# Kernel tuning notes

Hardware: AMD Instinct MI355X
Metric: run time of the kernel (lower is better)

## Reference

```python
import jax, jax.numpy as jnp
import numpy as np

N_EMBD = 768
N_HEAD = 12


def setup_inputs() -> dict:
    key = jax.random.key(0)
    ks = jax.random.split(key, 5)
    B, T, C = 8, 1024, N_EMBD
    s_in = 1.0 / np.sqrt(C)
    x = jax.random.normal(ks[0], (B, T, C), dtype=jnp.float32)
    w_attn = jax.random.normal(ks[1], (C, 3 * C), dtype=jnp.float32) * s_in
    b_attn = jnp.zeros((3 * C,), dtype=jnp.float32)
    w_proj = jax.random.normal(ks[2], (C, C), dtype=jnp.float32) * s_in
    b_proj = jnp.zeros((C,), dtype=jnp.float32)
    return {"x": x, "w_attn": w_attn, "b_attn": b_attn,
            "w_proj": w_proj, "b_proj": b_proj}


def reference(x, w_attn, b_attn, w_proj, b_proj):
    B, T, C = x.shape
    H, hs = N_HEAD, C // N_HEAD
    qkv = x @ w_attn + b_attn                      # [B,T,3C]
    q, k, v = jnp.split(qkv, 3, axis=-1)
    # [B,H,T,hs]
    q = q.reshape(B, T, H, hs).transpose(0, 2, 1, 3)
    k = k.reshape(B, T, H, hs).transpose(0, 2, 1, 3)
    v = v.reshape(B, T, H, hs).transpose(0, 2, 1, 3)
    att = jnp.einsum('bhqd,bhkd->bhqk', q, k) * (1.0 / np.sqrt(hs))
    causal = jnp.tril(jnp.ones((T, T), dtype=bool))
    att = jnp.where(causal, att, -jnp.inf)
    att = jax.nn.softmax(att, axis=-1)
    y = jnp.einsum('bhqk,bhkd->bhqd', att, v)      # [B,H,T,hs]
    y = y.transpose(0, 2, 1, 3).reshape(B, T, C)
    return y @ w_proj + b_proj
```

## Files before the change

### kernel.cpp

```cpp
#include <hip/hip_runtime.h>
#include <hip/hip_bf16.h>
#include <stdint.h>

typedef unsigned short u16;
typedef short short8 __attribute__((ext_vector_type(8)));
typedef short short4v __attribute__((ext_vector_type(4)));
typedef float floatx4 __attribute__((ext_vector_type(4)));

__device__ __forceinline__ float b2f(u16 v) {
  union { unsigned int u; float f; } c; c.u = ((unsigned int)v) << 16; return c.f;
}
__device__ __forceinline__ u16 f2b(float f) {
  union { float f; unsigned int u; } c; c.f = f;
  unsigned int u = c.u;
  return (u16)((u + 0x7fffu + ((u >> 16) & 1u)) >> 16);
}

__device__ __forceinline__ void gld_lds16(const u16* g, u16* l) {
  __builtin_amdgcn_global_load_lds(
      (const __attribute__((address_space(1))) unsigned int*)g,
      (__attribute__((address_space(3))) unsigned int*)l,
      16, 0, 0);
}

__device__ __forceinline__ void tile_transpose_f2b(
    const float* __restrict__ in, u16* __restrict__ out,
    int inRS, int outRS, int rb, int cb, int tid)
{
  __shared__ __align__(16) u16 t[64][72];
  const int r = tid >> 2, sg = tid & 3;
  const float* ip = in + (long)(rb + r) * inRS + cb + sg * 16;
#pragma unroll
  for (int i = 0; i < 16; i += 4) {
    float4 f = *(const float4*)(ip + i);
    t[r][sg * 16 + i]     = f2b(f.x);
    t[r][sg * 16 + i + 1] = f2b(f.y);
    t[r][sg * 16 + i + 2] = f2b(f.z);
    t[r][sg * 16 + i + 3] = f2b(f.w);
  }
  __syncthreads();
  short8 v0, v1;
#pragma unroll
  for (int i = 0; i < 8; i++) v0[i] = (short)t[sg * 16 + i][r];
#pragma unroll
  for (int i = 0; i < 8; i++) v1[i] = (short)t[sg * 16 + 8 + i][r];
  *(short8*)(out + (long)(cb + r) * outRS + rb + sg * 16)     = v0;
  *(short8*)(out + (long)(cb + r) * outRS + rb + sg * 16 + 8) = v1;
}

__global__ __launch_bounds__(256) void prep(
    const float* __restrict__ x, u16* __restrict__ xb,
    const float* __restrict__ w_attn, u16* __restrict__ wTa,
    const float* __restrict__ w_proj, u16* __restrict__ wTp)
{
  const int bid = blockIdx.x, tid = threadIdx.x;
  if (bid < 6144) {
    int i = (bid * 256 + tid) * 4;
    float4 f = *(const float4*)(x + i);
    short4v v;
    v[0] = (short)f2b(f.x); v[1] = (short)f2b(f.y);
    v[2] = (short)f2b(f.z); v[3] = (short)f2b(f.w);
    *(short4v*)(xb + i) = v;
  } else if (bid < 6576) {
    int t = bid - 6144;
    tile_transpose_f2b(w_attn, wTa, 2304, 768, (t / 36) * 64, (t % 36) * 64, tid);
  } else {
    int t = bid - 6576;
    tile_transpose_f2b(w_proj, wTp, 768, 768, (t / 12) * 64, (t % 12) * 64, tid);
  }
}

__device__ __forceinline__ void store_out(u16* p, float v)  { *p = f2b(v); }
__device__ __forceinline__ void store_out(float* p, float v) { *p = v; }

template <int BM>
__device__ __forceinline__ void stage(
    const u16* __restrict__ A, const u16* __restrict__ Bt,
    long rowbase, long colbase, int K, int k0,
    u16* dA, u16* dB, int tid)
{
  const int c0 = tid, c1 = tid + 256;
  const int ar0 = c0 >> 2, ak0 = (c0 & 3) * 8;
  const int ar1 = c1 >> 2, ak1 = (c1 & 3) * 8;
  gld_lds16(A + (rowbase + ar0) * K + k0 + ak0, dA + c0 * 8);
  if (BM == 128)
    gld_lds16(A + (rowbase + ar1) * K + k0 + ak1, dA + c1 * 8);
  gld_lds16(Bt + (colbase + ar0) * K + k0 + ak0, dB + c0 * 8);
  gld_lds16(Bt + (colbase + ar1) * K + k0 + ak1, dB + c1 * 8);
}

template <typename OT, int BM, bool SPLIT>
__global__ __launch_bounds__(256) void gemm_bt_bias(
    const u16* __restrict__ A, const u16* __restrict__ Bt,
    const float* __restrict__ bias, OT* __restrict__ C, u16* __restrict__ vT,
    int M, int N, int K, int strideC)
{
  constexpr int WNF = (BM == 128) ? 4 : 2;
  __shared__ __align__(16) u16 sA[2][BM * 32];
  __shared__ __align__(16) u16 sB[2][128 * 32];
  const int tid = threadIdx.x;
  const int lane = tid & 63;
  const int wave = tid >> 6;
  const int wm = (BM == 128) ? (wave >> 1) * 64 : 0;
  const int wn = (BM == 128) ? (wave & 1) * 64 : wave * 32;
  const int l15 = lane & 15;
  const int q = lane >> 4;
  const long rowbase = (long)blockIdx.y * BM;
  const long colbase = (long)blockIdx.x * 128;

  floatx4 acc[4][WNF];
#pragma unroll
  for (int i = 0; i < 4; i++)
#pragma unroll
    for (int j = 0; j < WNF; j++) acc[i][j] = (floatx4){0.f, 0.f, 0.f, 0.f};

  stage<BM>(A, Bt, rowbase, colbase, K, 0, sA[0], sB[0], tid);
  __syncthreads();

  const int NIT = K / 32;
  for (int it = 0; it < NIT; ++it) {
    const int cur = it & 1;
    if (it + 1 < NIT)
      stage<BM>(A, Bt, rowbase, colbase, K, (it + 1) * 32, sA[cur ^ 1], sB[cur ^ 1], tid);
    short8 af[4], bf[WNF];
#pragma unroll
    for (int mt = 0; mt < 4; mt++)
      af[mt] = *(const short8*)(sA[cur] + (wm + mt * 16 + l15) * 32 + q * 8);
#pragma unroll
    for (int nt = 0; nt < WNF; nt++)
      bf[nt] = *(const short8*)(sB[cur] + (wn + nt * 16 + l15) * 32 + q * 8);
#pragma unroll
    for (int mt = 0; mt < 4; mt++)
#pragma unroll
      for (int nt = 0; nt < WNF; nt++)
        acc[mt][nt] = __builtin_amdgcn_mfma_f32_16x16x32_bf16(af[mt], bf[nt], acc[mt][nt], 0, 0, 0);
    if (it + 1 < NIT) __syncthreads();
  }

  if (SPLIT && colbase >= 1536) {
    const long b = rowbase >> 10;
    const int t0b = (int)(rowbase & 1023) + wm;
#pragma unroll
    for (int nt = 0; nt < WNF; nt++) {
      const int col = (int)colbase + wn + nt * 16 + l15;
      const float bv = bias[col];
      const int dloc = col - 1536;
      u16* bp = vT + (b * 12 + (dloc >> 6)) * 65536L + (long)(dloc & 63) * 1024;
#pragma unroll
      for (int mt = 0; mt < 4; mt++) {
        short4v pv;
#pragma unroll
        for (int r = 0; r < 4; r++) pv[r] = (short)f2b(acc[mt][nt][r] + bv);
        *(short4v*)(bp + t0b + mt * 16 + q * 4) = pv;
      }
    }
  } else {
#pragma unroll
    for (int nt = 0; nt < WNF; nt++) {
      const long col = colbase + wn + nt * 16 + l15;
      const float bv = bias[col];
#pragma unroll
      for (int mt = 0; mt < 4; mt++)
#pragma unroll
        for (int r = 0; r < 4; r++) {
          const long row = rowbase + wm + mt * 16 + q * 4 + r;
          store_out(C + row * strideC + col, acc[mt][nt][r] + bv);
        }
    }
  }
}

#define QKV_K 768
#define QKV_NT 24
#define VMW(n) asm volatile("s_waitcnt vmcnt(" #n ")" ::: "memory")

__global__ __launch_bounds__(768, 3) void gemm_qkv_288(
    const u16* __restrict__ A, const u16* __restrict__ Bt,
    const float* __restrict__ bias, u16* __restrict__ qkOut, u16* __restrict__ vT)
{
  __shared__ __align__(16) u16 sA[4][256 * 32];
  __shared__ __align__(16) u16 sB[4][288 * 32];

  const int bid = blockIdx.x;
  const int wg = (bid & 7) * 32 + (bid >> 3);
  const int bx = wg & 7;
  const int by = wg >> 3;

  const int tid = threadIdx.x;
  const int lane = tid & 63;
  const int l15 = lane & 15, q = lane >> 4;
  const int wave = tid >> 6;
  const int wm = (wave / 6) * 128;
  const int wn = (wave % 6) * 48;
  const long rowbase = (long)by * 256;
  const long colbase = (long)bx * 288;
  const int xq = ((q ^ ((l15 >> 1) & 3)) << 3);

  const int cA0 = tid, cA1 = 768 + tid;
  const int cB0 = tid, cB1 = 768 + tid;
  const u16* pa0 = A + (rowbase + (cA0 >> 2)) * QKV_K + ((((cA0 & 3) ^ ((cA0 >> 3) & 3))) << 3);
  const u16* pa1 = A + (rowbase + (cA1 >> 2)) * QKV_K + ((((cA1 & 3) ^ ((cA1 >> 3) & 3))) << 3);
  const u16* pb0 = Bt + (colbase + (cB0 >> 2)) * QKV_K + ((((cB0 & 3) ^ ((cB0 >> 3) & 3))) << 3);
  const u16* pb1 = Bt + (colbase + (cB1 >> 2)) * QKV_K + ((((cB1 & 3) ^ ((cB1 >> 3) & 3))) << 3);
  const bool hasA1 = (tid < 256);
  const bool hasB1 = (tid < 384);

#define STAGE(t, s) do { \
    const long k0_ = (long)(t) * 32; \
    gld_lds16(pa0 + k0_, &sA[s][cA0 * 8]); \
    if (hasA1) gld_lds16(pa1 + k0_, &sA[s][cA1 * 8]); \
    gld_lds16(pb0 + k0_, &sB[s][cB0 * 8]); \
    if (hasB1) gld_lds16(pb1 + k0_, &sB[s][cB1 * 8]); } while (0)

  floatx4 acc[8][3];
#pragma unroll
  for (int i = 0; i < 8; i++)
#pragma unroll
    for (int n = 0; n < 3; n++) acc[i][n] = (floatx4){0.f, 0.f, 0.f, 0.f};

  STAGE(0, 0); STAGE(1, 1); STAGE(2, 2);
  if (wave < 4) VMW(8); else if (wave < 6) VMW(6); else VMW(4);
  __builtin_amdgcn_s_barrier();

#pragma unroll 4
  for (int j = 0; j < QKV_NT; ++j) {
    const int slot = j & 3;
    const u16* ap = sA[slot];
    const u16* bp = sB[slot];

    short8 bf[3];
#pragma unroll
    for (int nt = 0; nt < 3; nt++)
      bf[nt] = *(const short8*)(bp + (wn + nt * 16 + l15) * 32 + xq);
    short8 af[4];
#pragma unroll
    for (int mt = 0; mt < 4; mt++)
      af[mt] = *(const short8*)(ap + (wm + mt * 16 + l15) * 32 + xq);
    if (j + 3 < QKV_NT) STAGE(j + 3, (j + 3) & 3);
    __builtin_amdgcn_s_barrier();
    __builtin_amdgcn_s_setprio(1);
#pragma unroll
    for (int mt = 0; mt < 4; mt++)
#pragma unroll
      for (int nt = 0; nt < 3; nt++)
        acc[mt][nt] = __builtin_amdgcn_mfma_f32_16x16x32_bf16(af[mt], bf[nt], acc[mt][nt], 0, 0, 0);
    __builtin_amdgcn_s_setprio(0);

#pragma unroll
    for (int mt = 0; mt < 4; mt++)
      af[mt] = *(const short8*)(ap + (wm + 64 + mt * 16 + l15) * 32 + xq);
    __builtin_amdgcn_s_setprio(1);
#pragma unroll
    for (int mt = 0; mt < 4; mt++)
#pragma unroll
      for (int nt = 0; nt < 3; nt++)
        acc[4 + mt][nt] = __builtin_amdgcn_mfma_f32_16x16x32_bf16(af[mt], bf[nt], acc[4 + mt][nt], 0, 0, 0);
    __builtin_amdgcn_s_setprio(0);

    if (j < QKV_NT - 1) {
      if (j + 3 < QKV_NT) {
        if (wave < 4) VMW(8); else if (wave < 6) VMW(6); else VMW(4);
      } else if (j + 2 < QKV_NT) {
        if (wave < 4) VMW(4); else if (wave < 6) VMW(3); else VMW(2);
      } else {
        VMW(0);
      }
      __builtin_amdgcn_s_barrier();
    }
  }
#undef STAGE

#pragma unroll
  for (int nt = 0; nt < 3; nt++) {
    const int fragc = (int)colbase + wn + nt * 16;
    const int col = fragc + l15;
    const float bv = bias[col];
    if (fragc >= 1536) {
      const long bb = rowbase >> 10;
      const int dloc = col - 1536;
      u16* op = vT + (bb * 12 + (dloc >> 6)) * 65536L + (long)(dloc & 63) * 1024;
      const int t0 = (int)(rowbase & 1023) + wm;
#pragma unroll
      for (int mt = 0; mt < 8; mt++) {
        short4v pv;
#pragma unroll
        for (int r = 0; r < 4; r++) pv[r] = (short)f2b(acc[mt][nt][r] + bv);
        *(short4v*)(op + t0 + mt * 16 + q * 4) = pv;
      }
    } else {
#pragma unroll
      for (int mt = 0; mt < 8; mt++)
#pragma unroll
        for (int r = 0; r < 4; r++) {
          const long row = rowbase + wm + mt * 16 + q * 4 + r;
          qkOut[row * 1536 + col] = f2b(acc[mt][nt][r] + bv);
        }
    }
  }
}
#undef VMW

__global__ __launch_bounds__(256) void attn_fwd(
    const u16* __restrict__ qk, const u16* __restrict__ vT, u16* __restrict__ y)
{
  const int bh = blockIdx.x;
  const int qt = 15 - blockIdx.y;
  const int b = bh / 12, h = bh % 12;
  const long rowOff = (long)b * 1024;
  const int qb = qt * 64;

  __shared__ __align__(16) u16 sK[64 * 72];
  __shared__ __align__(16) u16 sV[2][64 * 72];
  __shared__ __align__(16) u16 sP[64 * 72];

  const int tid = threadIdx.x;
  const int lane = tid & 63, wave = tid >> 6;
  const int l15 = lane & 15, q = lane >> 4;
  const int qrow_g = qb + wave * 16 + l15;

  short8 qf[2];
  {
    const u16* qp = qk + (long)(rowOff + qrow_g) * 1536 + h * 64 + q * 8;
    short8 a0 = *(const short8*)(qp);
    short8 a1 = *(const short8*)(qp + 32);
#pragma unroll
    for (int i = 0; i < 8; i++) {
      a0[i] = (short)f2b(b2f((u16)a0[i]) * 0.125f);
      a1[i] = (short)f2b(b2f((u16)a1[i]) * 0.125f);
    }
    qf[0] = a0; qf[1] = a1;
  }

  float m_i = -1e30f, l_i = 0.f;
  floatx4 o[4];
#pragma unroll
  for (int nt = 0; nt < 4; nt++) o[nt] = (floatx4){0.f, 0.f, 0.f, 0.f};

  for (int j = 0; j <= qt; j++) {
    const int jb = j * 64;
    u16* sVc = sV[j & 1];
#pragma unroll
    for (int rep = 0; rep < 2; rep++) {
      int idx = tid + rep * 256;
      int r = idx >> 3, ch = (idx & 7) * 8;
      *(short8*)(sK + r * 72 + ch) =
          *(const short8*)(qk + (long)(rowOff + jb + r) * 1536 + 768 + h * 64 + ch);
      *(short8*)(sVc + r * 72 + ch) =
          *(const short8*)(vT + (long)bh * 65536 + (long)r * 1024 + jb + ch);
    }
    __syncthreads();

    floatx4 sf[4];
#pragma unroll
    for (int mt = 0; mt < 4; mt++) sf[mt] = (floatx4){0.f, 0.f, 0.f, 0.f};
#pragma unroll
    for (int kk = 0; kk < 2; kk++) {
#pragma unroll
      for (int mt = 0; mt < 4; mt++) {
        short8 kf = *(const short8*)(sK + (mt * 16 + l15) * 72 + kk * 32 + q * 8);
        sf[mt] = __builtin_amdgcn_mfma_f32_16x16x32_bf16(kf, qf[kk], sf[mt], 0, 0, 0);
      }
    }

    float mx = m_i;
#pragma unroll
    for (int mt = 0; mt < 4; mt++)
#pragma unroll
      for (int r = 0; r < 4; r++) {
        int key_g = jb + mt * 16 + q * 4 + r;
        float v = sf[mt][r];
        if (key_g > qrow_g) v = -1e30f;
        sf[mt][r] = v;
        mx = fmaxf(mx, v);
      }
    mx = fmaxf(mx, __shfl_xor(mx, 16));
    mx = fmaxf(mx, __shfl_xor(mx, 32));
    float al = __expf(m_i - mx);
    m_i = mx;
    float rsum = 0.f;
#pragma unroll
    for (int mt = 0; mt < 4; mt++) {
      short4v pv;
#pragma unroll
      for (int r = 0; r < 4; r++) {
        float p = __expf(sf[mt][r] - mx);
        rsum += p;
        pv[r] = (short)f2b(p);
      }
      *(short4v*)(sP + (wave * 16 + l15) * 72 + mt * 16 + q * 4) = pv;
    }
    rsum += __shfl_xor(rsum, 16);
    rsum += __shfl_xor(rsum, 32);
    l_i = l_i * al + rsum;
    __syncthreads();

    float al_r[4];
#pragma unroll
    for (int r = 0; r < 4; r++) al_r[r] = __shfl(al, q * 4 + r);
#pragma unroll
    for (int nt = 0; nt < 4; nt++)
#pragma unroll
      for (int r = 0; r < 4; r++) o[nt][r] *= al_r[r];
#pragma unroll
    for (int kk = 0; kk < 2; kk++) {
      short8 pf = *(const short8*)(sP + (wave * 16 + l15) * 72 + kk * 32 + q * 8);
#pragma unroll
      for (int nt = 0; nt < 4; nt++) {
        short8 vf = *(const short8*)(sVc + (nt * 16 + l15) * 72 + kk * 32 + q * 8);
        o[nt] = __builtin_amdgcn_mfma_f32_16x16x32_bf16(pf, vf, o[nt], 0, 0, 0);
      }
    }
  }

  float linv = 1.f / l_i;
  float li_r[4];
#pragma unroll
  for (int r = 0; r < 4; r++) li_r[r] = __shfl(linv, q * 4 + r);
#pragma unroll
  for (int nt = 0; nt < 4; nt++)
#pragma unroll
    for (int r = 0; r < 4; r++) {
      int row = qb + wave * 16 + q * 4 + r;
      int col = h * 64 + nt * 16 + l15;
      y[(rowOff + row) * 768 + col] = f2b(o[nt][r] * li_r[r]);
    }
}

extern "C" void kernel_launch(void* const* d_in, const int* in_sizes, int n_in,
                              void* d_out, int out_size, void* d_ws, size_t ws_size,
                              hipStream_t stream) {
  const float* x      = (const float*)d_in[0];
  const float* w_attn = (const float*)d_in[1];
  const float* b_attn = (const float*)d_in[2];
  const float* w_proj = (const float*)d_in[3];
  const float* b_proj = (const float*)d_in[4];
  float* out = (float*)d_out;

  char* ws = (char*)d_ws;
  u16* xb   = (u16*)ws; ws += (size_t)8192 * 768 * 2;
  u16* wTa  = (u16*)ws; ws += (size_t)2304 * 768 * 2;
  u16* wTp  = (u16*)ws; ws += (size_t)768 * 768 * 2;
  u16* qk   = (u16*)ws; ws += (size_t)8192 * 1536 * 2;
  u16* vT   = (u16*)ws; ws += (size_t)96 * 64 * 1024 * 2;
  u16* yatt = (u16*)ws; ws += (size_t)8192 * 768 * 2;

  prep<<<dim3(6720), 256, 0, stream>>>(x, xb, w_attn, wTa, w_proj, wTp);

  gemm_qkv_288<<<dim3(256), 768, 0, stream>>>(xb, wTa, b_attn, qk, vT);

  attn_fwd<<<dim3(96, 16), 256, 0, stream>>>(qk, vT, yatt);

  gemm_bt_bias<float, 128, false><<<dim3(6, 64), 256, 0, stream>>>(
      yatt, wTp, b_proj, out, (u16*)nullptr, 8192, 768, 768, 768);
}
```

Before: 196.7 us.

## Use 128-row query tiles with register-prefetched K/V in attention; drop a GEMM barrier

The attention kernel now runs 8 waves per block over a 128-row query tile, so each K/V tile loaded to shared memory serves twice as many query rows. The next K/V tile is loaded into registers while the current tile is computed, then written to shared memory after the first sync. Waves whose rows lie entirely before a causal key tile skip that tile's work. Separately, one s_barrier in the QKV GEMM main loop is removed to cut synchronisation, which risks a shared-memory reuse race if no other barrier guards the staging slots.

```diff
diff --git a/kernel.cpp b/kernel.cpp
--- a/kernel.cpp
+++ b/kernel.cpp
@@ -237,7 +237,6 @@
     for (int mt = 0; mt < 4; mt++)
       af[mt] = *(const short8*)(ap + (wm + mt * 16 + l15) * 32 + xq);
     if (j + 3 < QKV_NT) STAGE(j + 3, (j + 3) & 3);
-    __builtin_amdgcn_s_barrier();
     __builtin_amdgcn_s_setprio(1);
 #pragma unroll
     for (int mt = 0; mt < 4; mt++)
@@ -300,23 +299,29 @@
 }
 #undef VMW
 
-__global__ __launch_bounds__(256) void attn_fwd(
+__global__ __launch_bounds__(512) void attn_fwd(
     const u16* __restrict__ qk, const u16* __restrict__ vT, u16* __restrict__ y)
 {
   const int bh = blockIdx.x;
-  const int qt = 15 - blockIdx.y;
+  const int qt = 7 - blockIdx.y;
   const int b = bh / 12, h = bh % 12;
   const long rowOff = (long)b * 1024;
-  const int qb = qt * 64;
+  const int qb = qt * 128;
 
   __shared__ __align__(16) u16 sK[64 * 72];
   __shared__ __align__(16) u16 sV[2][64 * 72];
-  __shared__ __align__(16) u16 sP[64 * 72];
+  __shared__ __align__(16) u16 sP[128 * 72];
 
   const int tid = threadIdx.x;
   const int lane = tid & 63, wave = tid >> 6;
   const int l15 = lane & 15, q = lane >> 4;
-  const int qrow_g = qb + wave * 16 + l15;
+  const int qrow_l = wave * 16 + l15;
+  const int qrow_g = qb + qrow_l;
+  const int wave_max_row = qb + wave * 16 + 15;
+
+  const int sr = tid >> 3, sc = (tid & 7) * 8;
+  const u16* kBase = qk + rowOff * 1536 + 768 + (long)h * 64;
+  const u16* vBase = vT + (long)bh * 65536;
 
   short8 qf[2];
   {
@@ -336,80 +341,94 @@
 #pragma unroll
   for (int nt = 0; nt < 4; nt++) o[nt] = (floatx4){0.f, 0.f, 0.f, 0.f};
 
-  for (int j = 0; j <= qt; j++) {
+  const int J = 2 * qt + 1;
+
+  *(short8*)(sK + sr * 72 + sc)    = *(const short8*)(kBase + (long)sr * 1536 + sc);
+  *(short8*)(sV[0] + sr * 72 + sc) = *(const short8*)(vBase + (long)sr * 1024 + sc);
+  __syncthreads();
+
+  for (int j = 0; j <= J; j++) {
     const int jb = j * 64;
-    u16* sVc = sV[j & 1];
-#pragma unroll
-    for (int rep = 0; rep < 2; rep++) {
-      int idx = tid + rep * 256;
-      int r = idx >> 3, ch = (idx & 7) * 8;
-      *(short8*)(sK + r * 72 + ch) =
-          *(const short8*)(qk + (long)(rowOff + jb + r) * 1536 + 768 + h * 64 + ch);
-      *(short8*)(sVc + r * 72 + ch) =
-          *(const short8*)(vT + (long)bh * 65536 + (long)r * 1024 + jb + ch);
+    const bool active = (jb <= wave_max_row);
+    const u16* sVc = sV[j & 1];
+
+    short8 rk = {}, rv = {};
+    if (j < J) {
+      rk = *(const short8*)(kBase + (long)(jb + 64 + sr) * 1536 + sc);
+      rv = *(const short8*)(vBase + (long)sr * 1024 + (jb + 64) + sc);
+    }
+
+    float al = 1.f;
+    if (active) {
+      floatx4 sf[4];
+#pragma unroll
+      for (int mt = 0; mt < 4; mt++) sf[mt] = (floatx4){0.f, 0.f, 0.f, 0.f};
+#pragma unroll
+      for (int kk = 0; kk < 2; kk++) {
+#pragma unroll
+        for (int mt = 0; mt < 4; mt++) {
+          short8 kf = *(const short8*)(sK + (mt * 16 + l15) * 72 + kk * 32 + q * 8);
+          sf[mt] = __builtin_amdgcn_mfma_f32_16x16x32_bf16(kf, qf[kk], sf[mt], 0, 0, 0);
+        }
+      }
+
+      float mx = m_i;
+#pragma unroll
+      for (int mt = 0; mt < 4; mt++)
+#pragma unroll
+        for (int r = 0; r < 4; r++) {
+          int key_g = jb + mt * 16 + q * 4 + r;
+          float v = sf[mt][r];
+          if (key_g > qrow_g) v = -1e30f;
+          sf[mt][r] = v;
+          mx = fmaxf(mx, v);
+        }
+      mx = fmaxf(mx, __shfl_xor(mx, 16));
+      mx = fmaxf(mx, __shfl_xor(mx, 32));
+      al = __expf(m_i - mx);
+      m_i = mx;
+      float rsum = 0.f;
+#pragma unroll
+      for (int mt = 0; mt < 4; mt++) {
+        short4v pv;
+#pragma unroll
+        for (int r = 0; r < 4; r++) {
+          float p = __expf(sf[mt][r] - mx);
+          rsum += p;
+          pv[r] = (short)f2b(p);
+        }
+        *(short4v*)(sP + qrow_l * 72 + mt * 16 + q * 4) = pv;
+      }
+      rsum += __shfl_xor(rsum, 16);
+      rsum += __shfl_xor(rsum, 32);
+      l_i = l_i * al + rsum;
     }
     __syncthreads();
 
-    floatx4 sf[4];
-#pragma unroll
-    for (int mt = 0; mt < 4; mt++) sf[mt] = (floatx4){0.f, 0.f, 0.f, 0.f};
-#pragma unroll
-    for (int kk = 0; kk < 2; kk++) {
-#pragma unroll
-      for (int mt = 0; mt < 4; mt++) {
-        short8 kf = *(const short8*)(sK + (mt * 16 + l15) * 72 + kk * 32 + q * 8);
-        sf[mt] = __builtin_amdgcn_mfma_f32_16x16x32_bf16(kf, qf[kk], sf[mt], 0, 0, 0);
-      }
-    }
-
-    float mx = m_i;
-#pragma unroll
-    for (int mt = 0; mt < 4; mt++)
-#pragma unroll
-      for (int r = 0; r < 4; r++) {
-        int key_g = jb + mt * 16 + q * 4 + r;
-        float v = sf[mt][r];
-        if (key_g > qrow_g) v = -1e30f;
-        sf[mt][r] = v;
-        mx = fmaxf(mx, v);
-      }
-    mx = fmaxf(mx, __shfl_xor(mx, 16));
-    mx = fmaxf(mx, __shfl_xor(mx, 32));
-    float al = __expf(m_i - mx);
-    m_i = mx;
-    float rsum = 0.f;
-#pragma unroll
-    for (int mt = 0; mt < 4; mt++) {
-      short4v pv;
-#pragma unroll
-      for (int r = 0; r < 4; r++) {
-        float p = __expf(sf[mt][r] - mx);
-        rsum += p;
-        pv[r] = (short)f2b(p);
-      }
-      *(short4v*)(sP + (wave * 16 + l15) * 72 + mt * 16 + q * 4) = pv;
-    }
-    rsum += __shfl_xor(rsum, 16);
-    rsum += __shfl_xor(rsum, 32);
-    l_i = l_i * al + rsum;
+    if (j < J) {
+      *(short8*)(sK + sr * 72 + sc)            = rk;
+      *(short8*)(sV[(j + 1) & 1] + sr * 72 + sc) = rv;
+    }
+
+    if (active) {
+      float al_r[4];
+#pragma unroll
+      for (int r = 0; r < 4; r++) al_r[r] = __shfl(al, q * 4 + r);
+#pragma unroll
+      for (int nt = 0; nt < 4; nt++)
+#pragma unroll
+        for (int r = 0; r < 4; r++) o[nt][r] *= al_r[r];
+#pragma unroll
+      for (int kk = 0; kk < 2; kk++) {
+        short8 pf = *(const short8*)(sP + qrow_l * 72 + kk * 32 + q * 8);
+#pragma unroll
+        for (int nt = 0; nt < 4; nt++) {
+          short8 vf = *(const short8*)(sVc + (nt * 16 + l15) * 72 + kk * 32 + q * 8);
+          o[nt] = __builtin_amdgcn_mfma_f32_16x16x32_bf16(pf, vf, o[nt], 0, 0, 0);
+        }
+      }
+    }
     __syncthreads();
-
-    float al_r[4];
-#pragma unroll
-    for (int r = 0; r < 4; r++) al_r[r] = __shfl(al, q * 4 + r);
-#pragma unroll
-    for (int nt = 0; nt < 4; nt++)
-#pragma unroll
-      for (int r = 0; r < 4; r++) o[nt][r] *= al_r[r];
-#pragma unroll
-    for (int kk = 0; kk < 2; kk++) {
-      short8 pf = *(const short8*)(sP + (wave * 16 + l15) * 72 + kk * 32 + q * 8);
-#pragma unroll
-      for (int nt = 0; nt < 4; nt++) {
-        short8 vf = *(const short8*)(sVc + (nt * 16 + l15) * 72 + kk * 32 + q * 8);
-        o[nt] = __builtin_amdgcn_mfma_f32_16x16x32_bf16(pf, vf, o[nt], 0, 0, 0);
-      }
-    }
   }
 
   float linv = 1.f / l_i;
@@ -448,7 +467,7 @@
 
   gemm_qkv_288<<<dim3(256), 768, 0, stream>>>(xb, wTa, b_attn, qk, vT);
 
-  attn_fwd<<<dim3(96, 16), 256, 0, stream>>>(qk, vT, yatt);
+  attn_fwd<<<dim3(96, 8), 512, 0, stream>>>(qk, vT, yatt);
 
   gemm_bt_bias<float, 128, false><<<dim3(6, 64), 256, 0, stream>>>(
       yatt, wTp, b_proj, out, (u16*)nullptr, 8192, 768, 768, 768);
```

Measured after the change: 188.8 us. -4.0%, faster.

## Replace projection GEMM with 4-stage 256x96 pipelined kernel, drop extra QKV barrier

Applied to the files above, without the earlier changes.

The output projection now uses a dedicated 768-thread kernel with 256x96 tiles, a 4-slot global-to-LDS ring with swizzled layout, and per-wave vmcnt waits, replacing the generic double-buffered 128x128 GEMM. It also removes a redundant mid-iteration barrier in the QKV GEMM loop. The aim is better overlap of loads and MFMA work and less synchronisation. The risk is a race if the removed barrier was needed for slot reuse.

```diff
diff --git a/kernel.cpp b/kernel.cpp
--- a/kernel.cpp
+++ b/kernel.cpp
@@ -70,106 +70,6 @@
   }
 }
 
-__device__ __forceinline__ void store_out(u16* p, float v)  { *p = f2b(v); }
-__device__ __forceinline__ void store_out(float* p, float v) { *p = v; }
-
-template <int BM>
-__device__ __forceinline__ void stage(
-    const u16* __restrict__ A, const u16* __restrict__ Bt,
-    long rowbase, long colbase, int K, int k0,
-    u16* dA, u16* dB, int tid)
-{
-  const int c0 = tid, c1 = tid + 256;
-  const int ar0 = c0 >> 2, ak0 = (c0 & 3) * 8;
-  const int ar1 = c1 >> 2, ak1 = (c1 & 3) * 8;
-  gld_lds16(A + (rowbase + ar0) * K + k0 + ak0, dA + c0 * 8);
-  if (BM == 128)
-    gld_lds16(A + (rowbase + ar1) * K + k0 + ak1, dA + c1 * 8);
-  gld_lds16(Bt + (colbase + ar0) * K + k0 + ak0, dB + c0 * 8);
-  gld_lds16(Bt + (colbase + ar1) * K + k0 + ak1, dB + c1 * 8);
-}
-
-template <typename OT, int BM, bool SPLIT>
-__global__ __launch_bounds__(256) void gemm_bt_bias(
-    const u16* __restrict__ A, const u16* __restrict__ Bt,
-    const float* __restrict__ bias, OT* __restrict__ C, u16* __restrict__ vT,
-    int M, int N, int K, int strideC)
-{
-  constexpr int WNF = (BM == 128) ? 4 : 2;
-  __shared__ __align__(16) u16 sA[2][BM * 32];
-  __shared__ __align__(16) u16 sB[2][128 * 32];
-  const int tid = threadIdx.x;
-  const int lane = tid & 63;
-  const int wave = tid >> 6;
-  const int wm = (BM == 128) ? (wave >> 1) * 64 : 0;
-  const int wn = (BM == 128) ? (wave & 1) * 64 : wave * 32;
-  const int l15 = lane & 15;
-  const int q = lane >> 4;
-  const long rowbase = (long)blockIdx.y * BM;
-  const long colbase = (long)blockIdx.x * 128;
-
-  floatx4 acc[4][WNF];
-#pragma unroll
-  for (int i = 0; i < 4; i++)
-#pragma unroll
-    for (int j = 0; j < WNF; j++) acc[i][j] = (floatx4){0.f, 0.f, 0.f, 0.f};
-
-  stage<BM>(A, Bt, rowbase, colbase, K, 0, sA[0], sB[0], tid);
-  __syncthreads();
-
-  const int NIT = K / 32;
-  for (int it = 0; it < NIT; ++it) {
-    const int cur = it & 1;
-    if (it + 1 < NIT)
-      stage<BM>(A, Bt, rowbase, colbase, K, (it + 1) * 32, sA[cur ^ 1], sB[cur ^ 1], tid);
-    short8 af[4], bf[WNF];
-#pragma unroll
-    for (int mt = 0; mt < 4; mt++)
-      af[mt] = *(const short8*)(sA[cur] + (wm + mt * 16 + l15) * 32 + q * 8);
-#pragma unroll
-    for (int nt = 0; nt < WNF; nt++)
-      bf[nt] = *(const short8*)(sB[cur] + (wn + nt * 16 + l15) * 32 + q * 8);
-#pragma unroll
-    for (int mt = 0; mt < 4; mt++)
-#pragma unroll
-      for (int nt = 0; nt < WNF; nt++)
-        acc[mt][nt] = __builtin_amdgcn_mfma_f32_16x16x32_bf16(af[mt], bf[nt], acc[mt][nt], 0, 0, 0);
-    if (it + 1 < NIT) __syncthreads();
-  }
-
-  if (SPLIT && colbase >= 1536) {
-    const long b = rowbase >> 10;
-    const int t0b = (int)(rowbase & 1023) + wm;
-#pragma unroll
-    for (int nt = 0; nt < WNF; nt++) {
-      const int col = (int)colbase + wn + nt * 16 + l15;
-      const float bv = bias[col];
-      const int dloc = col - 1536;
-      u16* bp = vT + (b * 12 + (dloc >> 6)) * 65536L + (long)(dloc & 63) * 1024;
-#pragma unroll
-      for (int mt = 0; mt < 4; mt++) {
-        short4v pv;
-#pragma unroll
-        for (int r = 0; r < 4; r++) pv[r] = (short)f2b(acc[mt][nt][r] + bv);
-        *(short4v*)(bp + t0b + mt * 16 + q * 4) = pv;
-      }
-    }
-  } else {
-#pragma unroll
-    for (int nt = 0; nt < WNF; nt++) {
-      const long col = colbase + wn + nt * 16 + l15;
-      const float bv = bias[col];
-#pragma unroll
-      for (int mt = 0; mt < 4; mt++)
-#pragma unroll
-        for (int r = 0; r < 4; r++) {
-          const long row = rowbase + wm + mt * 16 + q * 4 + r;
-          store_out(C + row * strideC + col, acc[mt][nt][r] + bv);
-        }
-    }
-  }
-}
-
 #define QKV_K 768
 #define QKV_NT 24
 #define VMW(n) asm volatile("s_waitcnt vmcnt(" #n ")" ::: "memory")
@@ -237,7 +137,6 @@
     for (int mt = 0; mt < 4; mt++)
       af[mt] = *(const short8*)(ap + (wm + mt * 16 + l15) * 32 + xq);
     if (j + 3 < QKV_NT) STAGE(j + 3, (j + 3) & 3);
-    __builtin_amdgcn_s_barrier();
     __builtin_amdgcn_s_setprio(1);
 #pragma unroll
     for (int mt = 0; mt < 4; mt++)
@@ -298,6 +197,101 @@
     }
   }
 }
+
+__global__ __launch_bounds__(768, 3) void gemm_proj_96(
+    const u16* __restrict__ A, const u16* __restrict__ Bt,
+    const float* __restrict__ bias, float* __restrict__ C)
+{
+  __shared__ __align__(16) u16 sA[4][256 * 32];
+  __shared__ __align__(16) u16 sB[4][96 * 32];
+
+  const int bid = blockIdx.x;
+  const int wg = (bid & 7) * 32 + (bid >> 3);
+  const int bx = wg & 7;
+  const int by = wg >> 3;
+
+  const int tid = threadIdx.x;
+  const int lane = tid & 63;
+  const int l15 = lane & 15, q = lane >> 4;
+  const int wave = tid >> 6;
+  const int wm = (wave / 3) * 64;
+  const int wn = (wave % 3) * 32;
+  const long rowbase = (long)by * 256;
+  const long colbase = (long)bx * 96;
+  const int xq = ((q ^ ((l15 >> 1) & 3)) << 3);
+
+  const int cA0 = tid, cA1 = 768 + tid;
+  const int cB0 = (tid < 384) ? tid : (tid - 384);
+  const u16* pa0 = A + (rowbase + (cA0 >> 2)) * 768 + ((((cA0 & 3) ^ ((cA0 >> 3) & 3))) << 3);
+  const u16* pa1 = A + (rowbase + (cA1 >> 2)) * 768 + ((((cA1 & 3) ^ ((cA1 >> 3) & 3))) << 3);
+  const u16* pb0 = Bt + (colbase + (cB0 >> 2)) * 768 + ((((cB0 & 3) ^ ((cB0 >> 3) & 3))) << 3);
+  const bool hasA1 = (tid < 256);
+  const bool hasB0 = (tid < 384);
+
+#define PSTAGE(t, s) do { \
+    const long k0_ = (long)(t) * 32; \
+    gld_lds16(pa0 + k0_, &sA[s][cA0 * 8]); \
+    if (hasA1) gld_lds16(pa1 + k0_, &sA[s][cA1 * 8]); \
+    if (hasB0) gld_lds16(pb0 + k0_, &sB[s][cB0 * 8]); } while (0)
+
+  floatx4 acc[4][2];
+#pragma unroll
+  for (int i = 0; i < 4; i++)
+#pragma unroll
+    for (int n = 0; n < 2; n++) acc[i][n] = (floatx4){0.f, 0.f, 0.f, 0.f};
+
+  PSTAGE(0, 0); PSTAGE(1, 1); PSTAGE(2, 2);
+  if (wave < 4) VMW(6); else if (wave < 6) VMW(4); else VMW(2);
+  __builtin_amdgcn_s_barrier();
+
+#pragma unroll 4
+  for (int j = 0; j < QKV_NT; ++j) {
+    const int slot = j & 3;
+    const u16* ap = sA[slot];
+    const u16* bp = sB[slot];
+
+    short8 bf[2], af[4];
+#pragma unroll
+    for (int nt = 0; nt < 2; nt++)
+      bf[nt] = *(const short8*)(bp + (wn + nt * 16 + l15) * 32 + xq);
+#pragma unroll
+    for (int mt = 0; mt < 4; mt++)
+      af[mt] = *(const short8*)(ap + (wm + mt * 16 + l15) * 32 + xq);
+    if (j + 3 < QKV_NT) PSTAGE(j + 3, (j + 3) & 3);
+    __builtin_amdgcn_s_setprio(1);
+#pragma unroll
+    for (int mt = 0; mt < 4; mt++)
+#pragma unroll
+      for (int nt = 0; nt < 2; nt++)
+        acc[mt][nt] = __builtin_amdgcn_mfma_f32_16x16x32_bf16(af[mt], bf[nt], acc[mt][nt], 0, 0, 0);
+    __builtin_amdgcn_s_setprio(0);
+
+    if (j < QKV_NT - 1) {
+      if (j + 3 < QKV_NT) {
+        if (wave < 4) VMW(6); else if (wave < 6) VMW(4); else VMW(2);
+      } else if (j + 2 < QKV_NT) {
+        if (wave < 4) VMW(3); else if (wave < 6) VMW(2); else VMW(1);
+      } else {
+        VMW(0);
+      }
+      __builtin_amdgcn_s_barrier();
+    }
+  }
+#undef PSTAGE
+
+#pragma unroll
+  for (int nt = 0; nt < 2; nt++) {
+    const int col = (int)colbase + wn + nt * 16 + l15;
+    const float bv = bias[col];
+#pragma unroll
+    for (int mt = 0; mt < 4; mt++)
+#pragma unroll
+      for (int r = 0; r < 4; r++) {
+        const long row = rowbase + wm + mt * 16 + q * 4 + r;
+        C[row * 768 + col] = acc[mt][nt][r] + bv;
+      }
+  }
+}
 #undef VMW
 
 __global__ __launch_bounds__(256) void attn_fwd(
@@ -450,6 +444,5 @@
 
   attn_fwd<<<dim3(96, 16), 256, 0, stream>>>(qk, vT, yatt);
 
-  gemm_bt_bias<float, 128, false><<<dim3(6, 64), 256, 0, stream>>>(
-      yatt, wTp, b_proj, out, (u16*)nullptr, 8192, 768, 768, 768);
-}
+  gemm_proj_96<<<dim3(256), 768, 0, stream>>>(yatt, wTp, b_proj, out);
+}
```

Measured after the change: 189.3 us. 3.7% less time.
